# Performance work log

Hardware: AMD Instinct MI355X
Metric: run time of the kernel (lower is better)

Reference implementation:

```python
import jax, jax.numpy as jnp
import numpy as np
from itertools import combinations

SEQ_LEN = 10; WAY = 5; SHOT = 5; TSS = 2
IN_DIM = 2048; OUT_DIM = 2048
PAIRS = np.array(list(combinations(range(SEQ_LEN), TSS)))  # [T, 2] frame-pair indices
T = PAIRS.shape[0]  # 45 tuples


def _cdist(a, b):
    # Euclidean distance matrix, stable form: sqrt(|a|^2 + |b|^2 - 2 a.b)
    a2 = jnp.sum(a * a, axis=-1)[:, None]
    b2 = jnp.sum(b * b, axis=-1)[None, :]
    sq = a2 + b2 - 2.0 * (a @ b.T)
    return jnp.sqrt(jnp.maximum(sq, 0.0))


def setup_inputs() -> dict:
    key = jax.random.key(0)
    k1, k2, k3, k4 = jax.random.split(key, 4)
    n_s = WAY * SHOT            # 25
    n_q = WAY * 15              # 75
    support_set = jax.random.normal(k1, (n_s, SEQ_LEN, IN_DIM), jnp.float32)
    queries = jax.random.normal(k2, (n_q, SEQ_LEN, IN_DIM), jnp.float32)
    # class-sorted labels: class c occupies rows [c*SHOT, (c+1)*SHOT)
    support_labels = jnp.arange(n_s, dtype=jnp.int32) // SHOT
    lim = 1.0 / np.sqrt(IN_DIM * TSS)
    clsW_w = jax.random.uniform(k3, (OUT_DIM, IN_DIM * TSS), jnp.float32, -lim, lim)
    clsW_b = jax.random.uniform(k4, (OUT_DIM,), jnp.float32, -lim, lim)
    return {"support_set": support_set, "support_labels": support_labels,
            "queries": queries, "clsW_w": clsW_w, "clsW_b": clsW_b}


def _forward(support_set, queries, clsW_w, clsW_b):
    n_s, n_q = support_set.shape[0], queries.shape[0]
    D2 = TSS * IN_DIM
    # tuple gather: [n, T, 2*in_dim] (dropout is eval-mode identity)
    sup = support_set[:, PAIRS, :].reshape(n_s, T, D2)
    qry = queries[:, PAIRS, :].reshape(n_q, T, D2)
    q_embed = jax.nn.relu(qry.reshape(n_q * T, D2) @ clsW_w.T + clsW_b)      # [nqT, D]
    sup_c = sup.reshape(WAY, SHOT * T, D2)                                    # labels sorted by class
    support_all = jax.nn.relu(jnp.einsum('csd,od->cso', sup_c, clsW_w) + clsW_b)  # [way, sT, D]

    distmat = jax.vmap(lambda s: _cdist(q_embed, s))(support_all)             # [way, nqT, sT]
    # torch: view(-1, T, shot).topk(k=1, dim=1).mean -> max over reshaped axis
    dist_class = distmat.reshape(WAY, n_q * T, T, SHOT).max(axis=2)           # [way, nqT, shot]
    ave_dist_all = dist_class.mean(axis=2)                                    # [way, nqT]
    dist_min = distmat.min(axis=2).reshape(WAY, n_q, T).mean(axis=2).T        # [n_q, way] (computed, unused downstream)
    dist_max = distmat.max(axis=2).reshape(WAY, n_q, T).mean(axis=2).T        # [n_q, way]
    pos_all = jnp.argmax(distmat, axis=2)                                     # [way, nqT]

    cols = []
    for c in range(WAY):
        mse = support_all[c][pos_all[c]]                                      # [nqT, D]
        other = support_all[np.array([m for m in range(WAY) if m != c])]      # [way-1, sT, D]
        other_flat = other.reshape((WAY - 1) * SHOT * T, OUT_DIM)
        cosd = _cdist(mse, other_flat).reshape(n_q * T, WAY - 1, SHOT * T)
        cosd = cosd.transpose(1, 0, 2)                                        # [way-1, nqT, sT]
        # record_pos[idx, s2] = #{s1 : cosd[idx,s1,s2] > ave_dist_all[c, s1]}
        record = jnp.sum(cosd > ave_dist_all[c][None, :, None], axis=1).astype(jnp.float32)  # [way-1, sT]
        nz = jnp.maximum(jnp.sum(record != 0, axis=1), 1).astype(jnp.float32)
        thr = record.sum(axis=1) / nz                                         # mean over nonzero entries
        mask = (record < thr[:, None]).astype(jnp.float32)                    # selected columns per other-class
        # diff_embed = concat of selected rows; mean of cdist over them == masked mean
        d_full = _cdist(q_embed, other_flat)                                  # [nqT, (way-1)*sT]
        msum = jnp.maximum(mask.sum(), 1.0)
        mean_d = (d_full * mask.reshape(-1)[None, :]).sum(axis=1) / msum      # [nqT]
        cols.append(mean_d.reshape(n_q, T).mean(axis=1) / (WAY - 1))
    dist_contrast = jnp.stack(cols, axis=1)                                   # [n_q, way]

    logits_contrast = dist_max / (dist_contrast + dist_max)
    return dist_max, logits_contrast


def reference(support_set, support_labels, queries, clsW_w, clsW_b):
    # support_labels are sorted class blocks (arange // shot); class gather is a reshape
    return _forward(support_set, queries, clsW_w, clsW_b)
```

## Files before the change

kernel.cpp:

```cpp
#include <hip/hip_runtime.h>


typedef __bf16 bf16x8 __attribute__((ext_vector_type(8)));
typedef float f32x4 __attribute__((ext_vector_type(4)));

#define NQT   3375
#define MROWS 4500
#define MPAD  4608
#define LDD   1152
#define BK    32

__constant__ int P0[45] = {0,0,0,0,0,0,0,0,0,
                           1,1,1,1,1,1,1,1,
                           2,2,2,2,2,2,2,
                           3,3,3,3,3,3,
                           4,4,4,4,4,
                           5,5,5,5,
                           6,6,6,
                           7,7,
                           8};
__constant__ int P1[45] = {1,2,3,4,5,6,7,8,9,
                           2,3,4,5,6,7,8,9,
                           3,4,5,6,7,8,9,
                           4,5,6,7,8,9,
                           5,6,7,8,9,
                           6,7,8,9,
                           7,8,9,
                           8,9,
                           9};

__device__ inline unsigned short f2b(float x) {
  __bf16 b = (__bf16)x;
  return __builtin_bit_cast(unsigned short, b);
}
__device__ inline float b2f(unsigned int u16) {
  return __uint_as_float(u16 << 16);
}

__device__ __forceinline__ void gl_lds16(const unsigned short* g, unsigned short* l) {
  __builtin_amdgcn_global_load_lds(
      (__attribute__((address_space(1))) void*)(g),
      (__attribute__((address_space(3))) void*)(l),
      16, 0, 0);
}

__global__ void prep(const float* __restrict__ W, const float* __restrict__ Q,
                     const float* __restrict__ Sp,
                     unsigned short* __restrict__ Ws, unsigned short* __restrict__ X,
                     float* __restrict__ record, float* __restrict__ msum,
                     float* __restrict__ sq) {
  int b = blockIdx.x, tid = threadIdx.x;
  if (b < 8192) {
    int i = b * 256 + tid;
    int i4 = i << 2;
    int o  = i4 >> 12;
    int k  = i4 & 4095;
    int hf = k >> 11;
    int kk = k & 2047;
    float4 v = reinterpret_cast<const float4*>(W)[i];
    ushort4 u;
    u.x = f2b(v.x); u.y = f2b(v.y); u.z = f2b(v.z); u.w = f2b(v.w);
    *reinterpret_cast<ushort4*>(Ws + (size_t)(o + hf * 2048) * 2048 + kk) = u;
  } else if (b < 10240) {
    int i = (b - 8192) * 256 + tid;
    ushort4 u = {0, 0, 0, 0};
    if (i < 384000) {
      float4 v = reinterpret_cast<const float4*>(Q)[i];
      u.x = f2b(v.x); u.y = f2b(v.y); u.z = f2b(v.z); u.w = f2b(v.w);
    } else if (i < 512000) {
      float4 v = reinterpret_cast<const float4*>(Sp)[i - 384000];
      u.x = f2b(v.x); u.y = f2b(v.y); u.z = f2b(v.z); u.w = f2b(v.w);
    }
    reinterpret_cast<ushort4*>(X)[i] = u;
  } else {
    int i = (b - 10240) * 256 + tid;
    if (i < 4500) record[i] = 0.f;
    else if (i < 4505) msum[i - 4500] = 0.f;
    else if (i < 4505 + 4608) sq[i - 4505] = 0.f;
  }
}

__global__ __launch_bounds__(512)
void gemm_ring(const unsigned short* __restrict__ A, const unsigned short* __restrict__ B,
               int lda, int ldb, int Ksplit,
               float* __restrict__ Pout0, float* __restrict__ Pout1, int ldd) {
  __shared__ unsigned short As[3][128 * BK];
  __shared__ unsigned short Bs[3][128 * BK];
  const int tid  = threadIdx.x;
  const int wave = tid >> 6, lane = tid & 63;
  const int quad = lane >> 4, l16 = lane & 15;
  const int wm = (wave >> 2) * 64, wn = (wave & 3) * 32;
  const int m0 = blockIdx.x * 128, n0 = blockIdx.y * 128;
  const int kbase = blockIdx.z * Ksplit;

  f32x4 acc[4][2];
#pragma unroll
  for (int i = 0; i < 4; ++i)
#pragma unroll
    for (int j = 0; j < 2; ++j) {
      f32x4 z = {0.f, 0.f, 0.f, 0.f};
      acc[i][j] = z;
    }

  const int r0  = tid >> 2;
  const int qsw = (tid & 3) ^ ((tid >> 3) & 3);
  const int kp0 = qsw * 8;
  const int rsw = (quad ^ ((l16 >> 1) & 3)) * 8;
  const unsigned short* pa = A + (size_t)(m0 + r0) * lda + kbase + kp0;
  const unsigned short* pb = B + (size_t)(n0 + r0) * ldb + kbase + kp0;
  const int NKi = Ksplit / BK;

#define ISSUE(kk, st) do {                                 \
    gl_lds16(pa + (size_t)(kk) * BK, &As[st][wave * 512]); \
    gl_lds16(pb + (size_t)(kk) * BK, &Bs[st][wave * 512]); \
  } while (0)

  ISSUE(0, 0);
  ISSUE(1, 1);
  asm volatile("s_waitcnt vmcnt(2)" ::: "memory");
  __builtin_amdgcn_s_barrier();

  int sc = 0;
  for (int k = 0; k < NKi; ++k) {
    int sn = sc + 2; if (sn >= 3) sn -= 3;
    if (k + 2 < NKi) ISSUE(k + 2, sn);
    bf16x8 af[4], bfr[2];
#pragma unroll
    for (int t = 0; t < 4; ++t)
      af[t] = *reinterpret_cast<const bf16x8*>(&As[sc][(wm + t * 16 + l16) * BK + rsw]);
#pragma unroll
    for (int t = 0; t < 2; ++t)
      bfr[t] = *reinterpret_cast<const bf16x8*>(&Bs[sc][(wn + t * 16 + l16) * BK + rsw]);
#pragma unroll
    for (int i = 0; i < 4; ++i)
#pragma unroll
      for (int j = 0; j < 2; ++j)
        acc[i][j] = __builtin_amdgcn_mfma_f32_16x16x32_bf16(af[i], bfr[j], acc[i][j], 0, 0, 0);
    if (k + 1 < NKi) {
      if (k + 2 < NKi) asm volatile("s_waitcnt vmcnt(2)" ::: "memory");
      else             asm volatile("s_waitcnt vmcnt(0)" ::: "memory");
      __builtin_amdgcn_s_barrier();
    }
    sc = sc + 1; if (sc >= 3) sc = 0;
  }
#undef ISSUE
  asm volatile("s_waitcnt vmcnt(0)" ::: "memory");

  float* Pout = blockIdx.z ? Pout1 : Pout0;
#pragma unroll
  for (int i = 0; i < 4; ++i)
#pragma unroll
    for (int j = 0; j < 2; ++j) {
      int col = n0 + wn + j * 16 + l16;
      int rbase = m0 + wm + i * 16 + quad * 4;
      f32x4 v = acc[i][j];
#pragma unroll
      for (int r = 0; r < 4; ++r)
        Pout[(size_t)(rbase + r) * ldd + col] = v[r];
    }
}

__global__ __launch_bounds__(256)
void build_e2(const float* __restrict__ Y0, const float* __restrict__ Y1,
              const float* __restrict__ bias,
              unsigned short* __restrict__ E, float* __restrict__ sq) {
  int b = blockIdx.x, tid = threadIdx.x;
  if (b >= 400) {
    const size_t base = (size_t)4500 * 2048 / 8;
    const int total = 108 * 2048 / 8;
    uint4 z = {0, 0, 0, 0};
    for (int i = (b - 400) * 256 + tid; i < total; i += 512)
      reinterpret_cast<uint4*>(E)[base + i] = z;
    return;
  }
  int n = b >> 2, q = b & 3;
  int c0 = q * 512;
  __shared__ float Lf[10][512];
  __shared__ float Rf[10][512];
  for (int e = tid; e < 1280; e += 256) {
    int f  = e >> 7;
    int cc = (e & 127) << 2;
    const float* ya = Y0 + (size_t)(n * 10 + f) * 4096;
    const float* yb = Y1 + (size_t)(n * 10 + f) * 4096;
    float4 l0 = *reinterpret_cast<const float4*>(ya + c0 + cc);
    float4 l1 = *reinterpret_cast<const float4*>(yb + c0 + cc);
    float4 r0 = *reinterpret_cast<const float4*>(ya + 2048 + c0 + cc);
    float4 r1 = *reinterpret_cast<const float4*>(yb + 2048 + c0 + cc);
    float4 L = {l0.x + l1.x, l0.y + l1.y, l0.z + l1.z, l0.w + l1.w};
    float4 R = {r0.x + r1.x, r0.y + r1.y, r0.z + r1.z, r0.w + r1.w};
    *reinterpret_cast<float4*>(&Lf[f][cc]) = L;
    *reinterpret_cast<float4*>(&Rf[f][cc]) = R;
  }
  __syncthreads();
  int wv = tid >> 6, lane = tid & 63;
  int erow0 = (n < 75) ? n * 45 : NQT + (n - 75) * 45;
  for (int t = wv; t < 45; t += 4) {
    int f0 = P0[t], f1 = P1[t];
    int row = erow0 + t;
    float s = 0.f;
#pragma unroll
    for (int k = 0; k < 8; ++k) {
      int c = lane + 64 * k;
      float x = Lf[f0][c] + Rf[f1][c] + bias[c0 + c];
      x = fmaxf(x, 0.f);
      unsigned short ob = f2b(x);
      E[(size_t)row * 2048 + c0 + c] = ob;
      float xr = b2f(ob);
      s += xr * xr;
    }
#pragma unroll
    for (int sh = 32; sh > 0; sh >>= 1) s += __shfl_down(s, sh, 64);
    if (lane == 0) atomicAdd(&sq[row], s);
  }
}

__global__ __launch_bounds__(320)
void dist_stats(const float* __restrict__ Pa, const float* __restrict__ Pb,
                const float* __restrict__ sq, float* __restrict__ D,
                float* __restrict__ ave, int* __restrict__ pos,
                float* __restrict__ rmax) {
  __shared__ float drow[LDD];
  __shared__ float sm[5][64];
  int row = blockIdx.x, tid = threadIdx.x;
  float sr = sq[row];
  if (tid < 288) {
    int c = tid * 4;
    size_t ix = (size_t)row * LDD / 4 + tid;
    float4 a = reinterpret_cast<const float4*>(Pa)[ix];
    float4 bb = reinterpret_cast<const float4*>(Pb)[ix];
    float4 o;
    o.x = sqrtf(fmaxf(sr + sq[NQT + c + 0] - 2.f * (a.x + bb.x), 0.f));
    o.y = sqrtf(fmaxf(sr + sq[NQT + c + 1] - 2.f * (a.y + bb.y), 0.f));
    o.z = sqrtf(fmaxf(sr + sq[NQT + c + 2] - 2.f * (a.z + bb.z), 0.f));
    o.w = sqrtf(fmaxf(sr + sq[NQT + c + 3] - 2.f * (a.w + bb.w), 0.f));
    reinterpret_cast<float4*>(D)[ix] = o;
    *reinterpret_cast<float4*>(&drow[c]) = o;
  }
  __syncthreads();
  if (row >= NQT) return;
  int wv = tid >> 6, lane = tid & 63;
  const float* p = &drow[wv * 225];
  float best = -1e30f; int bi = 225;
  float gm = -1e30f;
  if (lane < 60) {
#pragma unroll
    for (int r = 0; r < 4; ++r) {
      int j = lane + 60 * r;
      if (j < 225) {
        float v = p[j];
        if (v > best) { best = v; bi = j; }
        gm = fmaxf(gm, v);
      }
    }
  }
#pragma unroll
  for (int s = 32; s > 0; s >>= 1) {
    float vv = __shfl_down(best, s, 64);
    int   ii = __shfl_down(bi,   s, 64);
    if (vv > best || (vv == best && ii < bi)) { best = vv; bi = ii; }
  }
  sm[wv][lane] = gm;
  __builtin_amdgcn_wave_barrier();
  if (lane < 5) {
    float m = -1e30f;
#pragma unroll
    for (int a = 0; a < 12; ++a) m = fmaxf(m, sm[wv][lane + 5 * a]);
    sm[wv][lane] = m;
  }
  __builtin_amdgcn_wave_barrier();
  if (lane == 0) {
    float s5 = sm[wv][0] + sm[wv][1] + sm[wv][2] + sm[wv][3] + sm[wv][4];
    ave[wv * NQT + row]  = s5 * 0.2f;
    pos[wv * NQT + row]  = bi;
    rmax[wv * NQT + row] = best;
  }
}

__global__ void record_part(const float* __restrict__ D, const float* __restrict__ ave,
                            const int* __restrict__ pos, float* __restrict__ record) {
  int b = blockIdx.x;
  int c = b / 135, chunk = b - c * 135;
  int i0 = chunk * 25;
  int tid = threadIdx.x;
  __shared__ int   sp[25];
  __shared__ float sa[25];
  if (tid < 25) {
    sp[tid] = pos[c * NQT + i0 + tid];
    sa[tid] = ave[c * NQT + i0 + tid];
  }
  __syncthreads();
  float cnt[4] = {0.f, 0.f, 0.f, 0.f};
  int gcol[4];
#pragma unroll
  for (int j = 0; j < 4; ++j) {
    int col = tid + j * 256;
    gcol[j] = (col < 900) ? (col < c * 225 ? col : col + 225) : 0;
  }
  const bool act3 = (tid + 768) < 900;
  const float* Dsup = D + (size_t)(NQT + c * 225) * LDD;
  for (int ii = 0; ii < 25; ++ii) {
    const float* row = Dsup + (size_t)sp[ii] * LDD;
    float a = sa[ii];
    cnt[0] += (row[gcol[0]] > a) ? 1.f : 0.f;
    cnt[1] += (row[gcol[1]] > a) ? 1.f : 0.f;
    cnt[2] += (row[gcol[2]] > a) ? 1.f : 0.f;
    if (act3) cnt[3] += (row[gcol[3]] > a) ? 1.f : 0.f;
  }
#pragma unroll
  for (int j = 0; j < 4; ++j) {
    int col = tid + j * 256;
    if (col < 900) atomicAdd(&record[c * 900 + col], cnt[j]);
  }
}

__global__ void record_finish(const float* __restrict__ record, float* __restrict__ mask,
                              float* __restrict__ msum) {
  int b = blockIdx.x;
  int c = b / 4, mi = b - c * 4;
  int tid = threadIdx.x;
  float r = (tid < 225) ? record[c * 900 + mi * 225 + tid] : 0.f;
  __shared__ float s1[256], s2[256];
  __shared__ float thr_s;
  s1[tid] = r;
  s2[tid] = (tid < 225 && r != 0.f) ? 1.f : 0.f;
  __syncthreads();
  for (int st = 128; st > 0; st >>= 1) {
    if (tid < st) { s1[tid] += s1[tid + st]; s2[tid] += s2[tid + st]; }
    __syncthreads();
  }
  if (tid == 0) {
    float nz = s2[0] < 1.f ? 1.f : s2[0];
    thr_s = s1[0] / nz;
  }
  __syncthreads();
  float m = 0.f;
  if (tid < 225) {
    m = (r < thr_s) ? 1.f : 0.f;
    mask[(c * 4 + mi) * 225 + tid] = m;
  }
  s1[tid] = m;
  __syncthreads();
  for (int st = 128; st > 0; st >>= 1) {
    if (tid < st) s1[tid] += s1[tid + st];
    __syncthreads();
  }
  if (tid == 0) atomicAdd(&msum[c], s1[0]);
}

__global__ __launch_bounds__(256)
void contrast_rows(const float* __restrict__ D, const float* __restrict__ mask,
                   float* __restrict__ S) {
  int wave = threadIdx.x >> 6, lane = threadIdx.x & 63;
  int i = blockIdx.x * 4 + wave;
  int c = blockIdx.y;
  if (i >= NQT) return;
  const float* row = D + (size_t)i * LDD;
  const float* mk  = mask + c * 900;
  const int cbase = c * 225;
  float acc = 0.f;
#pragma unroll
  for (int k = 0; k < 15; ++k) {
    int col = k * 64 + lane;
    if (col < 900) {
      int gcol = col + (col >= cbase ? 225 : 0);
      acc += mk[col] * row[gcol];
    }
  }
#pragma unroll
  for (int s = 32; s > 0; s >>= 1) acc += __shfl_down(acc, s, 64);
  if (lane == 0) S[c * NQT + i] = acc;
}

__global__ void final_kernel(const float* __restrict__ S, const float* __restrict__ msum,
                             const float* __restrict__ rmax, float* __restrict__ out) {
  int gid = blockIdx.x * 256 + threadIdx.x;
  if (gid >= 375) return;
  int q = gid / 5, c = gid - q * 5;
  float dsum = 0.f, ssum = 0.f;
  for (int t = 0; t < 45; ++t) {
    dsum += rmax[c * NQT + q * 45 + t];
    ssum += S[c * NQT + q * 45 + t];
  }
  float dm = dsum / 45.f;
  float ms = msum[c]; if (ms < 1.f) ms = 1.f;
  float contrast = ssum / (ms * 180.f);
  out[q * 5 + c] = dm;
  out[375 + q * 5 + c] = dm / (contrast + dm);
}

extern "C" void kernel_launch(void* const* d_in, const int* in_sizes, int n_in,
                              void* d_out, int out_size, void* d_ws, size_t ws_size,
                              hipStream_t stream) {
  const float* support = (const float*)d_in[0];
  const float* queries = (const float*)d_in[2];
  const float* W       = (const float*)d_in[3];
  const float* bias    = (const float*)d_in[4];
  float* out = (float*)d_out;

  char* ws = (char*)d_ws;
  size_t off = 0;
  unsigned short* Xb  = (unsigned short*)(ws + off);
  unsigned short* Wsp = (unsigned short*)(ws + off + 4194304);
  float*          Pd1 = (float*)(ws + off);          off += 21233664;
  float*          Y0  = (float*)(ws + off);          off += (size_t)1024 * 4096 * 4;
  float*          Dm  = (float*)(ws + off);
  float*          Y1  = (float*)(ws + off);          off += (size_t)MPAD * LDD * 4;
  unsigned short* Eb  = (unsigned short*)(ws + off); off += (size_t)MPAD * 2048 * 2;
  float* sq      = (float*)(ws + off); off += 4608 * 4 + 256;
  float* ave     = (float*)(ws + off); off += 5 * NQT * 4 + 256;
  int*   pos     = (int*)(ws + off);   off += 5 * NQT * 4 + 256;
  float* rmax    = (float*)(ws + off); off += 5 * NQT * 4 + 256;
  float* mask    = (float*)(ws + off); off += 5 * 4 * 225 * 4 + 256;
  float* record  = (float*)(ws + off); off += 5 * 900 * 4 + 256;
  float* Sbuf    = (float*)(ws + off); off += 5 * NQT * 4 + 256;
  float* msum    = (float*)(ws + off); off += 5 * 4 + 256;

  prep<<<10276, 256, 0, stream>>>(W, queries, support, Wsp, Xb, record, msum, sq);

  dim3 g1(1024 / 128, 4096 / 128, 2);
  gemm_ring<<<g1, 512, 0, stream>>>(Xb, Wsp, 2048, 2048, 1024, Y0, Y1, 4096);

  build_e2<<<402, 256, 0, stream>>>(Y0, Y1, bias, Eb, sq);

  dim3 g2(MPAD / 128, LDD / 128, 2);
  gemm_ring<<<g2, 512, 0, stream>>>(Eb, Eb + (size_t)NQT * 2048, 2048, 2048, 1024,
                                    Dm, Pd1, LDD);

  dist_stats<<<MROWS, 320, 0, stream>>>(Dm, Pd1, sq, Dm, ave, pos, rmax);

  record_part<<<675, 256, 0, stream>>>(Dm, ave, pos, record);
  record_finish<<<20, 256, 0, stream>>>(record, mask, msum);
  dim3 gc((NQT + 3) / 4, 5);
  contrast_rows<<<gc, 256, 0, stream>>>(Dm, mask, Sbuf);
  final_kernel<<<2, 256, 0, stream>>>(Sbuf, msum, rmax, out);
}
```

Before: 217.7 us.

## Double-step GEMM K loop with 4-stage ring; fuse per-class contrast into one pass

```diff
diff --git a/kernel.cpp b/kernel.cpp
--- a/kernel.cpp
+++ b/kernel.cpp
@@ -48,7 +48,7 @@
                      const float* __restrict__ Sp,
                      unsigned short* __restrict__ Ws, unsigned short* __restrict__ X,
                      float* __restrict__ record, float* __restrict__ msum,
-                     float* __restrict__ sq) {
+                     float* __restrict__ sq, float* __restrict__ maskT) {
   int b = blockIdx.x, tid = threadIdx.x;
   if (b < 8192) {
     int i = b * 256 + tid;
@@ -76,7 +76,8 @@
     int i = (b - 10240) * 256 + tid;
     if (i < 4500) record[i] = 0.f;
     else if (i < 4505) msum[i - 4500] = 0.f;
-    else if (i < 4505 + 4608) sq[i - 4505] = 0.f;
+    else if (i < 9113) sq[i - 4505] = 0.f;
+    else if (i < 14873) maskT[i - 9113] = 0.f;
   }
 }
 
@@ -84,8 +85,8 @@
 void gemm_ring(const unsigned short* __restrict__ A, const unsigned short* __restrict__ B,
                int lda, int ldb, int Ksplit,
                float* __restrict__ Pout0, float* __restrict__ Pout1, int ldd) {
-  __shared__ unsigned short As[3][128 * BK];
-  __shared__ unsigned short Bs[3][128 * BK];
+  __shared__ unsigned short As[4][128 * BK];
+  __shared__ unsigned short Bs[4][128 * BK];
   const int tid  = threadIdx.x;
   const int wave = tid >> 6, lane = tid & 63;
   const int quad = lane >> 4, l16 = lane & 15;
@@ -117,31 +118,40 @@
 
   ISSUE(0, 0);
   ISSUE(1, 1);
-  asm volatile("s_waitcnt vmcnt(2)" ::: "memory");
+  asm volatile("s_waitcnt vmcnt(0)" ::: "memory");
   __builtin_amdgcn_s_barrier();
 
-  int sc = 0;
-  for (int k = 0; k < NKi; ++k) {
-    int sn = sc + 2; if (sn >= 3) sn -= 3;
-    if (k + 2 < NKi) ISSUE(k + 2, sn);
-    bf16x8 af[4], bfr[2];
-#pragma unroll
-    for (int t = 0; t < 4; ++t)
-      af[t] = *reinterpret_cast<const bf16x8*>(&As[sc][(wm + t * 16 + l16) * BK + rsw]);
-#pragma unroll
-    for (int t = 0; t < 2; ++t)
-      bfr[t] = *reinterpret_cast<const bf16x8*>(&Bs[sc][(wn + t * 16 + l16) * BK + rsw]);
+  for (int kp = 0; kp < NKi; kp += 2) {
+    if (kp + 2 < NKi) {
+      ISSUE(kp + 2, (kp + 2) & 3);
+      ISSUE(kp + 3, (kp + 3) & 3);
+    }
+    const int s0 = kp & 3, s1 = s0 | 1;
+    bf16x8 a0[4], a1[4], b0[2], b1[2];
+#pragma unroll
+    for (int t = 0; t < 4; ++t) {
+      a0[t] = *reinterpret_cast<const bf16x8*>(&As[s0][(wm + t * 16 + l16) * BK + rsw]);
+      a1[t] = *reinterpret_cast<const bf16x8*>(&As[s1][(wm + t * 16 + l16) * BK + rsw]);
+    }
+#pragma unroll
+    for (int t = 0; t < 2; ++t) {
+      b0[t] = *reinterpret_cast<const bf16x8*>(&Bs[s0][(wn + t * 16 + l16) * BK + rsw]);
+      b1[t] = *reinterpret_cast<const bf16x8*>(&Bs[s1][(wn + t * 16 + l16) * BK + rsw]);
+    }
 #pragma unroll
     for (int i = 0; i < 4; ++i)
 #pragma unroll
       for (int j = 0; j < 2; ++j)
-        acc[i][j] = __builtin_amdgcn_mfma_f32_16x16x32_bf16(af[i], bfr[j], acc[i][j], 0, 0, 0);
-    if (k + 1 < NKi) {
-      if (k + 2 < NKi) asm volatile("s_waitcnt vmcnt(2)" ::: "memory");
-      else             asm volatile("s_waitcnt vmcnt(0)" ::: "memory");
+        acc[i][j] = __builtin_amdgcn_mfma_f32_16x16x32_bf16(a0[i], b0[j], acc[i][j], 0, 0, 0);
+#pragma unroll
+    for (int i = 0; i < 4; ++i)
+#pragma unroll
+      for (int j = 0; j < 2; ++j)
+        acc[i][j] = __builtin_amdgcn_mfma_f32_16x16x32_bf16(a1[i], b1[j], acc[i][j], 0, 0, 0);
+    if (kp + 2 < NKi) {
+      asm volatile("s_waitcnt vmcnt(0)" ::: "memory");
       __builtin_amdgcn_s_barrier();
     }
-    sc = sc + 1; if (sc >= 3) sc = 0;
   }
 #undef ISSUE
   asm volatile("s_waitcnt vmcnt(0)" ::: "memory");
@@ -313,7 +323,7 @@
   }
 }
 
-__global__ void record_finish(const float* __restrict__ record, float* __restrict__ mask,
+__global__ void record_finish(const float* __restrict__ record, float* __restrict__ maskT,
                               float* __restrict__ msum) {
   int b = blockIdx.x;
   int c = b / 4, mi = b - c * 4;
@@ -336,7 +346,9 @@
   float m = 0.f;
   if (tid < 225) {
     m = (r < thr_s) ? 1.f : 0.f;
-    mask[(c * 4 + mi) * 225 + tid] = m;
+    int L = mi * 225 + tid;
+    int g = L + (L >= c * 225 ? 225 : 0);
+    maskT[c * LDD + g] = m;
   }
   s1[tid] = m;
   __syncthreads();
@@ -348,27 +360,38 @@
 }
 
 __global__ __launch_bounds__(256)
-void contrast_rows(const float* __restrict__ D, const float* __restrict__ mask,
+void contrast_rows(const float* __restrict__ D, const float* __restrict__ maskT,
                    float* __restrict__ S) {
   int wave = threadIdx.x >> 6, lane = threadIdx.x & 63;
   int i = blockIdx.x * 4 + wave;
-  int c = blockIdx.y;
   if (i >= NQT) return;
   const float* row = D + (size_t)i * LDD;
-  const float* mk  = mask + c * 900;
-  const int cbase = c * 225;
-  float acc = 0.f;
-#pragma unroll
-  for (int k = 0; k < 15; ++k) {
+  float a0 = 0.f, a1 = 0.f, a2 = 0.f, a3 = 0.f, a4 = 0.f;
+#pragma unroll
+  for (int k = 0; k < 18; ++k) {
     int col = k * 64 + lane;
-    if (col < 900) {
-      int gcol = col + (col >= cbase ? 225 : 0);
-      acc += mk[col] * row[gcol];
-    }
-  }
-#pragma unroll
-  for (int s = 32; s > 0; s >>= 1) acc += __shfl_down(acc, s, 64);
-  if (lane == 0) S[c * NQT + i] = acc;
+    float d = row[col];
+    a0 += d * maskT[0 * LDD + col];
+    a1 += d * maskT[1 * LDD + col];
+    a2 += d * maskT[2 * LDD + col];
+    a3 += d * maskT[3 * LDD + col];
+    a4 += d * maskT[4 * LDD + col];
+  }
+#pragma unroll
+  for (int s = 32; s > 0; s >>= 1) {
+    a0 += __shfl_down(a0, s, 64);
+    a1 += __shfl_down(a1, s, 64);
+    a2 += __shfl_down(a2, s, 64);
+    a3 += __shfl_down(a3, s, 64);
+    a4 += __shfl_down(a4, s, 64);
+  }
+  if (lane == 0) {
+    S[0 * NQT + i] = a0;
+    S[1 * NQT + i] = a1;
+    S[2 * NQT + i] = a2;
+    S[3 * NQT + i] = a3;
+    S[4 * NQT + i] = a4;
+  }
 }
 
 __global__ void final_kernel(const float* __restrict__ S, const float* __restrict__ msum,
@@ -410,12 +433,12 @@
   float* ave     = (float*)(ws + off); off += 5 * NQT * 4 + 256;
   int*   pos     = (int*)(ws + off);   off += 5 * NQT * 4 + 256;
   float* rmax    = (float*)(ws + off); off += 5 * NQT * 4 + 256;
-  float* mask    = (float*)(ws + off); off += 5 * 4 * 225 * 4 + 256;
+  float* maskT   = (float*)(ws + off); off += 5 * LDD * 4 + 256;
   float* record  = (float*)(ws + off); off += 5 * 900 * 4 + 256;
   float* Sbuf    = (float*)(ws + off); off += 5 * NQT * 4 + 256;
   float* msum    = (float*)(ws + off); off += 5 * 4 + 256;
 
-  prep<<<10276, 256, 0, stream>>>(W, queries, support, Wsp, Xb, record, msum, sq);
+  prep<<<10299, 256, 0, stream>>>(W, queries, support, Wsp, Xb, record, msum, sq, maskT);
 
   dim3 g1(1024 / 128, 4096 / 128, 2);
   gemm_ring<<<g1, 512, 0, stream>>>(Xb, Wsp, 2048, 2048, 1024, Y0, Y1, 4096);
@@ -429,8 +452,7 @@
   dist_stats<<<MROWS, 320, 0, stream>>>(Dm, Pd1, sq, Dm, ave, pos, rmax);
 
   record_part<<<675, 256, 0, stream>>>(Dm, ave, pos, record);
-  record_finish<<<20, 256, 0, stream>>>(record, mask, msum);
-  dim3 gc((NQT + 3) / 4, 5);
-  contrast_rows<<<gc, 256, 0, stream>>>(Dm, mask, Sbuf);
+  record_finish<<<20, 256, 0, stream>>>(record, maskT, msum);
+  contrast_rows<<<(NQT + 3) / 4, 256, 0, stream>>>(Dm, maskT, Sbuf);
   final_kernel<<<2, 256, 0, stream>>>(Sbuf, msum, rmax, out);
 }
```

Result: no change. 217.4 us (-0.1%).

## Fuse mask/contrast/final tail into one kernel and deepen GEMM ring to four stages

Applied to the files above, without the earlier changes.

```diff
diff --git a/kernel.cpp b/kernel.cpp
--- a/kernel.cpp
+++ b/kernel.cpp
@@ -47,8 +47,7 @@
 __global__ void prep(const float* __restrict__ W, const float* __restrict__ Q,
                      const float* __restrict__ Sp,
                      unsigned short* __restrict__ Ws, unsigned short* __restrict__ X,
-                     float* __restrict__ record, float* __restrict__ msum,
-                     float* __restrict__ sq) {
+                     float* __restrict__ record, float* __restrict__ sq) {
   int b = blockIdx.x, tid = threadIdx.x;
   if (b < 8192) {
     int i = b * 256 + tid;
@@ -75,8 +74,7 @@
   } else {
     int i = (b - 10240) * 256 + tid;
     if (i < 4500) record[i] = 0.f;
-    else if (i < 4505) msum[i - 4500] = 0.f;
-    else if (i < 4505 + 4608) sq[i - 4505] = 0.f;
+    else if (i < 4500 + 4608) sq[i - 4500] = 0.f;
   }
 }
 
@@ -84,8 +82,8 @@
 void gemm_ring(const unsigned short* __restrict__ A, const unsigned short* __restrict__ B,
                int lda, int ldb, int Ksplit,
                float* __restrict__ Pout0, float* __restrict__ Pout1, int ldd) {
-  __shared__ unsigned short As[3][128 * BK];
-  __shared__ unsigned short Bs[3][128 * BK];
+  __shared__ unsigned short As[4][128 * BK];
+  __shared__ unsigned short Bs[4][128 * BK];
   const int tid  = threadIdx.x;
   const int wave = tid >> 6, lane = tid & 63;
   const int quad = lane >> 4, l16 = lane & 15;
@@ -117,13 +115,13 @@
 
   ISSUE(0, 0);
   ISSUE(1, 1);
-  asm volatile("s_waitcnt vmcnt(2)" ::: "memory");
+  ISSUE(2, 2);
+  asm volatile("s_waitcnt vmcnt(4)" ::: "memory");
   __builtin_amdgcn_s_barrier();
 
-  int sc = 0;
   for (int k = 0; k < NKi; ++k) {
-    int sn = sc + 2; if (sn >= 3) sn -= 3;
-    if (k + 2 < NKi) ISSUE(k + 2, sn);
+    if (k + 3 < NKi) ISSUE(k + 3, (k + 3) & 3);
+    const int sc = k & 3;
     bf16x8 af[4], bfr[2];
 #pragma unroll
     for (int t = 0; t < 4; ++t)
@@ -137,11 +135,11 @@
       for (int j = 0; j < 2; ++j)
         acc[i][j] = __builtin_amdgcn_mfma_f32_16x16x32_bf16(af[i], bfr[j], acc[i][j], 0, 0, 0);
     if (k + 1 < NKi) {
-      if (k + 2 < NKi) asm volatile("s_waitcnt vmcnt(2)" ::: "memory");
-      else             asm volatile("s_waitcnt vmcnt(0)" ::: "memory");
+      if (k + 3 < NKi)      asm volatile("s_waitcnt vmcnt(4)" ::: "memory");
+      else if (k + 2 < NKi) asm volatile("s_waitcnt vmcnt(2)" ::: "memory");
+      else                  asm volatile("s_waitcnt vmcnt(0)" ::: "memory");
       __builtin_amdgcn_s_barrier();
     }
-    sc = sc + 1; if (sc >= 3) sc = 0;
   }
 #undef ISSUE
   asm volatile("s_waitcnt vmcnt(0)" ::: "memory");
@@ -313,79 +311,97 @@
   }
 }
 
-__global__ void record_finish(const float* __restrict__ record, float* __restrict__ mask,
-                              float* __restrict__ msum) {
-  int b = blockIdx.x;
-  int c = b / 4, mi = b - c * 4;
+__global__ __launch_bounds__(256)
+void tail_fused(const float* __restrict__ D, const float* __restrict__ record,
+                const float* __restrict__ rmax, float* __restrict__ out) {
+  int q = blockIdx.x;
   int tid = threadIdx.x;
-  float r = (tid < 225) ? record[c * 900 + mi * 225 + tid] : 0.f;
-  __shared__ float s1[256], s2[256];
-  __shared__ float thr_s;
-  s1[tid] = r;
-  s2[tid] = (tid < 225 && r != 0.f) ? 1.f : 0.f;
-  __syncthreads();
-  for (int st = 128; st > 0; st >>= 1) {
-    if (tid < st) { s1[tid] += s1[tid + st]; s2[tid] += s2[tid + st]; }
-    __syncthreads();
-  }
-  if (tid == 0) {
-    float nz = s2[0] < 1.f ? 1.f : s2[0];
-    thr_s = s1[0] / nz;
-  }
-  __syncthreads();
-  float m = 0.f;
-  if (tid < 225) {
-    m = (r < thr_s) ? 1.f : 0.f;
-    mask[(c * 4 + mi) * 225 + tid] = m;
-  }
-  s1[tid] = m;
-  __syncthreads();
-  for (int st = 128; st > 0; st >>= 1) {
-    if (tid < st) s1[tid] += s1[tid + st];
-    __syncthreads();
-  }
-  if (tid == 0) atomicAdd(&msum[c], s1[0]);
-}
-
-__global__ __launch_bounds__(256)
-void contrast_rows(const float* __restrict__ D, const float* __restrict__ mask,
-                   float* __restrict__ S) {
-  int wave = threadIdx.x >> 6, lane = threadIdx.x & 63;
-  int i = blockIdx.x * 4 + wave;
-  int c = blockIdx.y;
-  if (i >= NQT) return;
-  const float* row = D + (size_t)i * LDD;
-  const float* mk  = mask + c * 900;
-  const int cbase = c * 225;
-  float acc = 0.f;
-#pragma unroll
-  for (int k = 0; k < 15; ++k) {
-    int col = k * 64 + lane;
-    if (col < 900) {
-      int gcol = col + (col >= cbase ? 225 : 0);
-      acc += mk[col] * row[gcol];
-    }
-  }
-#pragma unroll
-  for (int s = 32; s > 0; s >>= 1) acc += __shfl_down(acc, s, 64);
-  if (lane == 0) S[c * NQT + i] = acc;
-}
-
-__global__ void final_kernel(const float* __restrict__ S, const float* __restrict__ msum,
-                             const float* __restrict__ rmax, float* __restrict__ out) {
-  int gid = blockIdx.x * 256 + threadIdx.x;
-  if (gid >= 375) return;
-  int q = gid / 5, c = gid - q * 5;
-  float dsum = 0.f, ssum = 0.f;
-  for (int t = 0; t < 45; ++t) {
-    dsum += rmax[c * NQT + q * 45 + t];
-    ssum += S[c * NQT + q * 45 + t];
-  }
-  float dm = dsum / 45.f;
-  float ms = msum[c]; if (ms < 1.f) ms = 1.f;
-  float contrast = ssum / (ms * 180.f);
-  out[q * 5 + c] = dm;
-  out[375 + q * 5 + c] = dm / (contrast + dm);
+  int wv = tid >> 6, lane = tid & 63;
+  __shared__ float maskT[5 * LDD];
+  __shared__ float msum_s[5];
+  __shared__ float St[5][45];
+  for (int i = tid; i < 5 * LDD; i += 256) maskT[i] = 0.f;
+  if (tid < 5) msum_s[tid] = 0.f;
+  __syncthreads();
+
+  for (int seg = wv; seg < 20; seg += 4) {
+    int c = seg >> 2, mi = seg & 3;
+    const float* rec = record + c * 900 + mi * 225;
+    float r0 = (lane < 225) ? rec[lane] : 0.f;
+    float r1 = rec[lane + 64];
+    float r2 = rec[lane + 128];
+    float r3 = (lane + 192 < 225) ? rec[lane + 192] : 0.f;
+    float s  = r0 + r1 + r2 + r3;
+    float nz = (r0 != 0.f ? 1.f : 0.f) + (r1 != 0.f ? 1.f : 0.f) +
+               (r2 != 0.f ? 1.f : 0.f) + (r3 != 0.f ? 1.f : 0.f);
+#pragma unroll
+    for (int sh = 32; sh > 0; sh >>= 1) {
+      s  += __shfl_down(s,  sh, 64);
+      nz += __shfl_down(nz, sh, 64);
+    }
+    s  = __shfl(s,  0, 64);
+    nz = __shfl(nz, 0, 64);
+    float nzc = nz < 1.f ? 1.f : nz;
+    float thr = s / nzc;
+    float mcount = 0.f;
+    float rv[4] = {r0, r1, r2, r3};
+#pragma unroll
+    for (int j = 0; j < 4; ++j) {
+      int idx = lane + j * 64;
+      if (idx < 225) {
+        float m = (rv[j] < thr) ? 1.f : 0.f;
+        int L = mi * 225 + idx;
+        int g = L + (L >= c * 225 ? 225 : 0);
+        maskT[c * LDD + g] = m;
+        mcount += m;
+      }
+    }
+#pragma unroll
+    for (int sh = 32; sh > 0; sh >>= 1) mcount += __shfl_down(mcount, sh, 64);
+    if (lane == 0) atomicAdd(&msum_s[c], mcount);
+  }
+  __syncthreads();
+
+  for (int t = wv; t < 45; t += 4) {
+    const float* row = D + (size_t)(q * 45 + t) * LDD;
+    float a0 = 0.f, a1 = 0.f, a2 = 0.f, a3 = 0.f, a4 = 0.f;
+#pragma unroll
+    for (int k = 0; k < 18; ++k) {
+      int col = k * 64 + lane;
+      float d = row[col];
+      a0 += d * maskT[0 * LDD + col];
+      a1 += d * maskT[1 * LDD + col];
+      a2 += d * maskT[2 * LDD + col];
+      a3 += d * maskT[3 * LDD + col];
+      a4 += d * maskT[4 * LDD + col];
+    }
+#pragma unroll
+    for (int sh = 32; sh > 0; sh >>= 1) {
+      a0 += __shfl_down(a0, sh, 64);
+      a1 += __shfl_down(a1, sh, 64);
+      a2 += __shfl_down(a2, sh, 64);
+      a3 += __shfl_down(a3, sh, 64);
+      a4 += __shfl_down(a4, sh, 64);
+    }
+    if (lane == 0) {
+      St[0][t] = a0; St[1][t] = a1; St[2][t] = a2; St[3][t] = a3; St[4][t] = a4;
+    }
+  }
+  __syncthreads();
+
+  if (tid < 5) {
+    int c = tid;
+    float dsum = 0.f, ssum = 0.f;
+    for (int t = 0; t < 45; ++t) {
+      dsum += rmax[c * NQT + q * 45 + t];
+      ssum += St[c][t];
+    }
+    float dm = dsum / 45.f;
+    float ms = msum_s[c]; if (ms < 1.f) ms = 1.f;
+    float contrast = ssum / (ms * 180.f);
+    out[q * 5 + c] = dm;
+    out[375 + q * 5 + c] = dm / (contrast + dm);
+  }
 }
 
 extern "C" void kernel_launch(void* const* d_in, const int* in_sizes, int n_in,
@@ -410,12 +426,9 @@
   float* ave     = (float*)(ws + off); off += 5 * NQT * 4 + 256;
   int*   pos     = (int*)(ws + off);   off += 5 * NQT * 4 + 256;
   float* rmax    = (float*)(ws + off); off += 5 * NQT * 4 + 256;
-  float* mask    = (float*)(ws + off); off += 5 * 4 * 225 * 4 + 256;
   float* record  = (float*)(ws + off); off += 5 * 900 * 4 + 256;
-  float* Sbuf    = (float*)(ws + off); off += 5 * NQT * 4 + 256;
-  float* msum    = (float*)(ws + off); off += 5 * 4 + 256;
-
-  prep<<<10276, 256, 0, stream>>>(W, queries, support, Wsp, Xb, record, msum, sq);
+
+  prep<<<10276, 256, 0, stream>>>(W, queries, support, Wsp, Xb, record, sq);
 
   dim3 g1(1024 / 128, 4096 / 128, 2);
   gemm_ring<<<g1, 512, 0, stream>>>(Xb, Wsp, 2048, 2048, 1024, Y0, Y1, 4096);
@@ -429,8 +442,5 @@
   dist_stats<<<MROWS, 320, 0, stream>>>(Dm, Pd1, sq, Dm, ave, pos, rmax);
 
   record_part<<<675, 256, 0, stream>>>(Dm, ave, pos, record);
-  record_finish<<<20, 256, 0, stream>>>(record, mask, msum);
-  dim3 gc((NQT + 3) / 4, 5);
-  contrast_rows<<<gc, 256, 0, stream>>>(Dm, mask, Sbuf);
-  final_kernel<<<2, 256, 0, stream>>>(Sbuf, msum, rmax, out);
-}
+  tail_fused<<<75, 256, 0, stream>>>(Dm, record, rmax, out);
+}
```

After: 228.8 us. 1.05x slower.
